# Kernel optimization log

Hardware: AMD Instinct MI355X
Metric: run time of the kernel (lower is better)

The kernel has to match this reference:

```python
import jax, jax.numpy as jnp
import numpy as np

N = 4096        # number of target nodes (also attention key length)
K = 10          # num_neighbors
E = 128         # embedding_dimension
EF = 64         # edge_feature_dim
T = 64          # time_encoding_dim
H = 2           # num_attention_heads
D = E + T       # query_dim = 192
KEY = E + EF + T            # per-neighbor key dim = 256
KD = KEY * K                # flattened kdim/vdim = 2560


def setup_inputs() -> dict:
    key = jax.random.key(0)
    ks = jax.random.split(key, 16)
    s = 0.02
    return {
        "features": jax.random.normal(ks[0], (N, E), jnp.float32),
        "edge_feats": jax.random.normal(ks[1], (N, K, EF), jnp.float32),
        "time_feats": jax.random.normal(ks[2], (N, K, T), jnp.float32),
        "neighbors": jax.random.randint(ks[3], (N, K), 0, N),
        "node_idx": jnp.arange(N),
        # MultiheadAttention projections (jax convention: x @ W + b, W is [in, out])
        "Wq": jax.random.normal(ks[4], (D, D), jnp.float32) * s,
        "bq": jnp.zeros((D,), jnp.float32),
        "Wk": jax.random.normal(ks[5], (KD, D), jnp.float32) * s,
        "bk": jnp.zeros((D,), jnp.float32),
        "Wv": jax.random.normal(ks[6], (KD, D), jnp.float32) * s,
        "bv": jnp.zeros((D,), jnp.float32),
        "Wo": jax.random.normal(ks[7], (D, D), jnp.float32) * s,
        "bo": jnp.zeros((D,), jnp.float32),
        # MLP([query_dim + embedding, embedding, embedding]) with ReLU between layers
        "W1": jax.random.normal(ks[8], (D + E, E), jnp.float32) * s,
        "b1": jnp.zeros((E,), jnp.float32),
        "W2": jax.random.normal(ks[9], (E, E), jnp.float32) * s,
        "b2": jnp.zeros((E,), jnp.float32),
    }


def reference(features, edge_feats, time_feats, neighbors, node_idx,
              Wq, bq, Wk, bk, Wv, bv, Wo, bo, W1, b1, W2, b2):
    n, k = neighbors.shape
    hd = D // H
    # _aggregate: gather neighbor node features, concat edge + time feats, flatten
    neigh = features[neighbors]                                       # [N, K, E]
    agg = jnp.concatenate([neigh, edge_feats, time_feats], axis=-1)   # [N, K, KEY]
    agg = agg.reshape(n, k * KEY)                                     # [N, KD]
    # query: node features padded with zero time encoding
    x = features[node_idx]                                            # [N, E]
    q_in = jnp.concatenate([x, jnp.zeros((n, T), features.dtype)], axis=-1)  # [N, D]
    # multi-head attention: batch=1, every query attends over all N aggregated keys
    q = (q_in @ Wq + bq).reshape(n, H, hd)
    kk = (agg @ Wk + bk).reshape(n, H, hd)
    vv = (agg @ Wv + bv).reshape(n, H, hd)
    scale = 1.0 / jnp.sqrt(jnp.asarray(hd, features.dtype))
    scores = jnp.einsum('nhd,mhd->hnm', q, kk) * scale                # [H, N, N]
    attn = jax.nn.softmax(scores, axis=-1)
    o = jnp.einsum('hnm,mhd->nhd', attn, vv).reshape(n, D)
    attn_out = o @ Wo + bo                                            # [N, D]
    # MLP over concat(node_feats, attn_out)
    h = jnp.concatenate([x, attn_out], axis=-1)                       # [N, D+E]
    return jax.nn.relu(h @ W1 + b1) @ W2 + b2                         # [N, E]
```

## Files before the change

kernel.cpp:

```cpp
#include <hip/hip_runtime.h>
#include <hip/hip_bf16.h>
#include <math.h>

#define NN   4096
#define KNB  10
#define ED   128
#define EFD  64
#define TD   64
#define DD   192
#define KEYD 256
#define KDD  2560
#define HD   96
#define NH   2
#define NSPLIT 4

typedef __attribute__((ext_vector_type(8))) short bf16x8;
typedef __attribute__((ext_vector_type(4))) float f32x4;
typedef __attribute__((ext_vector_type(2))) unsigned int u32x2;

__device__ inline short f2bf(float f) {
    union { float f; unsigned int u; } c; c.f = f;
    unsigned int r = (c.u + 0x7FFFu + ((c.u >> 16) & 1u)) >> 16;
    return (short)r;
}

__device__ inline float bf2f(short s) {
    union { unsigned int u; float f; } c;
    c.u = ((unsigned int)(unsigned short)s) << 16;
    return c.f;
}

__device__ inline void gload_lds16(const void* g, void* lds) {
    __builtin_amdgcn_global_load_lds(
        (const __attribute__((address_space(1))) void*)g,
        (__attribute__((address_space(3))) void*)lds, 16, 0, 0);
}

__global__ __launch_bounds__(256) void prep_convert(
    const float* __restrict__ Wk, const float* __restrict__ Wv,
    const float* __restrict__ Wq,
    const float* __restrict__ Wo, const float* __restrict__ bo,
    const float* __restrict__ W1, const float* __restrict__ b1,
    const float* __restrict__ W2,
    const float* __restrict__ features, const float* __restrict__ edge_feats,
    const float* __restrict__ time_feats, const int* __restrict__ node_idx,
    short* __restrict__ WkT, short* __restrict__ WvT, short* __restrict__ WqT,
    short* __restrict__ WcatT, short* __restrict__ W2T, float* __restrict__ bfold,
    short* __restrict__ featbf, short* __restrict__ xb,
    short* __restrict__ edgebf, short* __restrict__ timebf)
{
    int blk = blockIdx.x, t = threadIdx.x;
    if (blk < 254) {
        __shared__ float ts[64][65];
        const float* W; short* WT; int src_ld, dst_ld, k0, n0;
        if (blk < 240) {
            int z = blk / 120, r = blk % 120;
            W = z ? Wv : Wk; WT = z ? WvT : WkT;
            src_ld = DD; dst_ld = KDD; k0 = (r % 40) * 64; n0 = (r / 40) * 64;
        } else if (blk < 246) {
            int r = blk - 240;
            W = Wq; WT = WqT; src_ld = DD; dst_ld = ED;
            k0 = (r % 2) * 64; n0 = (r / 2) * 64;
        } else if (blk < 250) {
            int r = blk - 246;
            W = W1; WT = WcatT; src_ld = ED; dst_ld = 320;
            k0 = (r % 2) * 64; n0 = (r / 2) * 64;
        } else {
            int r = blk - 250;
            W = W2; WT = W2T; src_ld = ED; dst_ld = ED;
            k0 = (r % 2) * 64; n0 = (r / 2) * 64;
        }
        #pragma unroll
        for (int j = 0; j < 4; ++j) {
            int k = (t >> 4) + j * 16, n4 = (t & 15) * 4;
            float4 v = *(const float4*)&W[(size_t)(k0 + k) * src_ld + n0 + n4];
            ts[k][n4] = v.x; ts[k][n4 + 1] = v.y; ts[k][n4 + 2] = v.z; ts[k][n4 + 3] = v.w;
        }
        __syncthreads();
        int n = t >> 2, kc = (t & 3) * 16;
        short tmp[16];
        #pragma unroll
        for (int j = 0; j < 16; ++j) tmp[j] = f2bf(ts[kc + j][n]);
        *(bf16x8*)&WT[(size_t)(n0 + n) * dst_ld + k0 + kc] = *(bf16x8*)&tmp[0];
        *(bf16x8*)&WT[(size_t)(n0 + n) * dst_ld + k0 + kc + 8] = *(bf16x8*)&tmp[8];
    } else if (blk == 254) {
        if (t < 128) {
            float s = 0.f;
            for (int j = 0; j < DD; ++j) s += bo[j] * W1[(size_t)(ED + j) * ED + t];
            bfold[t] = s + b1[t];
        }
    } else if (blk < 447) {
        int d = blk - 255;
        if (t < 128) {
            float s = 0.f;
            for (int j = 0; j < DD; ++j)
                s += Wo[(size_t)d * DD + j] * W1[(size_t)(ED + j) * ED + t];
            WcatT[t * 320 + ED + d] = f2bf(s);
        }
    } else {
        int cb = blk - 447;
        if (cb < 512) {
            int e4 = cb * 256 + t;
            float4 v = *(const float4*)&features[(size_t)e4 * 4];
            short4 o; o.x = f2bf(v.x); o.y = f2bf(v.y); o.z = f2bf(v.z); o.w = f2bf(v.w);
            *(short4*)&featbf[(size_t)e4 * 4] = o;
        } else if (cb < 1024) {
            int l4 = (cb - 512) * 256 + t;
            int n = l4 >> 5, c = (l4 & 31) * 4;
            float4 v = *(const float4*)&features[(size_t)node_idx[n] * ED + c];
            short4 o; o.x = f2bf(v.x); o.y = f2bf(v.y); o.z = f2bf(v.z); o.w = f2bf(v.w);
            *(short4*)&xb[(size_t)n * ED + c] = o;
        } else if (cb < 3584) {
            int l4 = (cb - 1024) * 256 + t;
            float4 v = *(const float4*)&edge_feats[(size_t)l4 * 4];
            short4 o; o.x = f2bf(v.x); o.y = f2bf(v.y); o.z = f2bf(v.z); o.w = f2bf(v.w);
            *(short4*)&edgebf[(size_t)l4 * 4] = o;
        } else {
            int l4 = (cb - 3584) * 256 + t;
            float4 v = *(const float4*)&time_feats[(size_t)l4 * 4];
            short4 o; o.x = f2bf(v.x); o.y = f2bf(v.y); o.z = f2bf(v.z); o.w = f2bf(v.w);
            *(short4*)&timebf[(size_t)l4 * 4] = o;
        }
    }
}

__global__ __launch_bounds__(256) void kvq_gemm_mfma(
    const short* __restrict__ featbf, const short* __restrict__ edgebf,
    const short* __restrict__ timebf, const int* __restrict__ neighbors,
    const short* __restrict__ WkT, const short* __restrict__ WvT,
    short* __restrict__ psumK, short* __restrict__ psumV,
    const short* __restrict__ xb, const short* __restrict__ WqT,
    const float* __restrict__ bq, short* __restrict__ qb)
{
    __shared__ short As[2][128 * 64];
    __shared__ short Bs[2][2][64 * 64];
    __shared__ unsigned short nbr[128 * KNB];
    int tid = threadIdx.x, wid = tid >> 6, lane = tid & 63;
    int lx = lane & 15, lg = lane >> 4;
    int id = blockIdx.x;

    if (id < 384) {
        int xcd = id & 7, slot_ = id >> 3;
        int g = xcd * 16 + slot_ / 3;
        int nb = slot_ % 3;
        int mb = g >> 2, s = g & 3;
        int n0 = nb * 64;
        int m0 = mb * 128;
        int wm0 = (wid >> 1) * 64, wn0 = (wid & 1) * 32;

        for (int i = tid; i < 128 * KNB; i += 256)
            nbr[i] = (unsigned short)neighbors[(size_t)m0 * KNB + i];
        __syncthreads();

        f32x4 accK[4][2] = {}, accV[4][2] = {};

        auto stage = [&](int k0, int b) {
            #pragma unroll
            for (int it = 0; it < 4; ++it) {
                int idx = (wid * 4 + it) * 64 + lane;
                int m = idx >> 3, cs = (idx & 7) ^ (m & 7);
                int k = k0 + cs * 8;
                int slot = k >> 8, off = k & 255;
                int nbid = nbr[m * KNB + slot];
                const short* src;
                if (off < ED)
                    src = featbf + (size_t)nbid * ED + off;
                else if (off < ED + EFD)
                    src = edgebf + ((size_t)(m0 + m) * KNB + slot) * EFD + (off - ED);
                else
                    src = timebf + ((size_t)(m0 + m) * KNB + slot) * TD + (off - ED - EFD);
                gload_lds16(src, &As[b][(wid * 4 + it) * 512]);
            }
            #pragma unroll
            for (int it = 0; it < 2; ++it) {
                int idx = (wid * 2 + it) * 64 + lane;
                int n = idx >> 3, c = (idx & 7) ^ (n & 7);
                gload_lds16(WkT + (size_t)(n0 + n) * KDD + k0 + c * 8,
                            &Bs[b][0][(wid * 2 + it) * 512]);
            }
            #pragma unroll
            for (int it = 0; it < 2; ++it) {
                int idx = (wid * 2 + it) * 64 + lane;
                int n = idx >> 3, c = (idx & 7) ^ (n & 7);
                gload_lds16(WvT + (size_t)(n0 + n) * KDD + k0 + c * 8,
                            &Bs[b][1][(wid * 2 + it) * 512]);
            }
        };

        int kbase = s * (KDD / NSPLIT);
        stage(kbase, 0);
        for (int i = 0; i < 10; ++i) {
            int b = i & 1;
            __syncthreads();
            if (i < 9) stage(kbase + (i + 1) * 64, b ^ 1);
            #pragma unroll
            for (int ks = 0; ks < 2; ++ks) {
                bf16x8 af[4], bk8[2], bv8[2];
                #pragma unroll
                for (int mf = 0; mf < 4; ++mf) {
                    int m = wm0 + mf * 16 + lx;
                    af[mf] = *(const bf16x8*)&As[b][m * 64 + (((ks * 4 + lg) ^ (m & 7)) << 3)];
                }
                #pragma unroll
                for (int nf = 0; nf < 2; ++nf) {
                    int n = wn0 + nf * 16 + lx;
                    int o = n * 64 + (((ks * 4 + lg) ^ (n & 7)) << 3);
                    bk8[nf] = *(const bf16x8*)&Bs[b][0][o];
                    bv8[nf] = *(const bf16x8*)&Bs[b][1][o];
                }
                #pragma unroll
                for (int mf = 0; mf < 4; ++mf)
                    #pragma unroll
                    for (int nf = 0; nf < 2; ++nf) {
                        accK[mf][nf] = __builtin_amdgcn_mfma_f32_16x16x32_bf16(
                            af[mf], bk8[nf], accK[mf][nf], 0, 0, 0);
                        accV[mf][nf] = __builtin_amdgcn_mfma_f32_16x16x32_bf16(
                            af[mf], bv8[nf], accV[mf][nf], 0, 0, 0);
                    }
            }
        }
        #pragma unroll
        for (int nf = 0; nf < 2; ++nf) {
            int ncol = n0 + wn0 + nf * 16 + lx;
            #pragma unroll
            for (int mf = 0; mf < 4; ++mf) {
                int mrow = m0 + wm0 + mf * 16 + 4 * lg;
                #pragma unroll
                for (int r = 0; r < 4; ++r)
                    psumK[((size_t)s * NN + mrow + r) * DD + ncol] = f2bf(accK[mf][nf][r]);
                short4 s4;
                s4.x = f2bf(accV[mf][nf][0]); s4.y = f2bf(accV[mf][nf][1]);
                s4.z = f2bf(accV[mf][nf][2]); s4.w = f2bf(accV[mf][nf][3]);
                *(short4*)&psumV[((size_t)(s * DD + ncol)) * NN + mrow] = s4;
            }
        }
    } else {
        int qid = id - 384;
        int m0 = (qid / 3) * 64, n0 = (qid % 3) * 64;
        int wm0 = (wid >> 1) * 32, wn0 = (wid & 1) * 32;
        short* qAs = &As[0][0];
        short* qBs = &Bs[0][0][0];
        f32x4 acc[2][2] = {};

        for (int k0 = 0; k0 < ED; k0 += 64) {
            #pragma unroll
            for (int it = 0; it < 2; ++it) {
                int idx = (wid * 2 + it) * 64 + lane;
                int m = idx >> 3, c = (idx & 7) ^ (m & 7);
                gload_lds16(xb + (size_t)(m0 + m) * ED + k0 + c * 8, &qAs[(wid * 2 + it) * 512]);
            }
            #pragma unroll
            for (int it = 0; it < 2; ++it) {
                int idx = (wid * 2 + it) * 64 + lane;
                int n = idx >> 3, c = (idx & 7) ^ (n & 7);
                gload_lds16(WqT + (size_t)(n0 + n) * ED + k0 + c * 8, &qBs[(wid * 2 + it) * 512]);
            }
            __syncthreads();
            #pragma unroll
            for (int ks = 0; ks < 2; ++ks) {
                bf16x8 af[2], bfr[2];
                #pragma unroll
                for (int mf = 0; mf < 2; ++mf) {
                    int m = wm0 + mf * 16 + lx;
                    af[mf] = *(const bf16x8*)&qAs[m * 64 + (((ks * 4 + lg) ^ (m & 7)) << 3)];
                }
                #pragma unroll
                for (int nf = 0; nf < 2; ++nf) {
                    int n = wn0 + nf * 16 + lx;
                    bfr[nf] = *(const bf16x8*)&qBs[n * 64 + (((ks * 4 + lg) ^ (n & 7)) << 3)];
                }
                #pragma unroll
                for (int mf = 0; mf < 2; ++mf)
                    #pragma unroll
                    for (int nf = 0; nf < 2; ++nf)
                        acc[mf][nf] = __builtin_amdgcn_mfma_f32_16x16x32_bf16(
                            af[mf], bfr[nf], acc[mf][nf], 0, 0, 0);
            }
            __syncthreads();
        }
        const float scale = 0.10206207261596577f;
        #pragma unroll
        for (int nf = 0; nf < 2; ++nf) {
            int ncol = n0 + wn0 + nf * 16 + lx;
            float bb = bq[ncol];
            #pragma unroll
            for (int mf = 0; mf < 2; ++mf) {
                int mrow = m0 + wm0 + mf * 16 + 4 * lg;
                #pragma unroll
                for (int r = 0; r < 4; ++r)
                    qb[(size_t)(mrow + r) * DD + ncol] = f2bf((acc[mf][nf][r] + bb) * scale);
            }
        }
    }
}

__global__ __launch_bounds__(256) void kv_combine(
    const short* __restrict__ psumK, const short* __restrict__ psumV,
    const float* __restrict__ bk, const float* __restrict__ bv,
    short* __restrict__ kk, short* __restrict__ vvT)
{
    const int HALF = NN * DD / 4;
    int i = blockIdx.x * 256 + threadIdx.x;
    if (i < HALF) {
        int base = i * 4, n = base % DD;
        float sum[4] = {0.f, 0.f, 0.f, 0.f};
        #pragma unroll
        for (int s = 0; s < NSPLIT; ++s) {
            short4 v = *(const short4*)&psumK[(size_t)s * NN * DD + base];
            sum[0] += bf2f(v.x); sum[1] += bf2f(v.y);
            sum[2] += bf2f(v.z); sum[3] += bf2f(v.w);
        }
        float4 bb = *(const float4*)&bk[n];
        short4 o;
        o.x = f2bf(sum[0] + bb.x); o.y = f2bf(sum[1] + bb.y);
        o.z = f2bf(sum[2] + bb.z); o.w = f2bf(sum[3] + bb.w);
        *(short4*)&kk[base] = o;
    } else {
        int j = i - HALF;
        int base = j * 4, n = base / NN;
        float sum[4] = {0.f, 0.f, 0.f, 0.f};
        #pragma unroll
        for (int s = 0; s < NSPLIT; ++s) {
            short4 v = *(const short4*)&psumV[(size_t)s * DD * NN + base];
            sum[0] += bf2f(v.x); sum[1] += bf2f(v.y);
            sum[2] += bf2f(v.z); sum[3] += bf2f(v.w);
        }
        float bb = bv[n];
        short4 o;
        o.x = f2bf(sum[0] + bb); o.y = f2bf(sum[1] + bb);
        o.z = f2bf(sum[2] + bb); o.w = f2bf(sum[3] + bb);
        *(short4*)&vvT[base] = o;
    }
}

__global__ __launch_bounds__(512) void attn_mfma(
    const short* __restrict__ qb,
    const short* __restrict__ kk,
    const short* __restrict__ vvT,
    short* __restrict__ opart,
    float* __restrict__ ml)
{
    __shared__ short Ks[2][64 * 96];
    __shared__ short Vs[2][96 * 64];
    __shared__ short Ps[8][16 * 72];
    int tid = threadIdx.x, wid = tid >> 6, lane = tid & 63;
    int lx = lane & 15, lg = lane >> 4;
    int h = blockIdx.y, split = blockIdx.z;
    int hoff = h * HD;
    int qb0 = blockIdx.x * 128 + wid * 16;

    bf16x8 qf[3];
    #pragma unroll
    for (int ks = 0; ks < 3; ++ks)
        qf[ks] = *(const bf16x8*)&qb[(size_t)(qb0 + lx) * DD + hoff + ks * 32 + lg * 8];

    auto stage = [&](int kb, int b) {
        #pragma unroll
        for (int jj = 0; jj < 3; ++jj) {
            int j = wid * 3 + jj;
            if (j < 12) {
                int idx = j * 64 + lane;
                int row = idx / 12, c = idx % 12;
                gload_lds16(kk + (size_t)(kb + row) * DD + hoff + c * 8,
                            &Ks[b][j * 512]);
            } else {
                int idx = (j - 12) * 64 + lane;
                int d = idx >> 3, c = (idx & 7) ^ (d & 7);
                gload_lds16(vvT + (size_t)(hoff + d) * NN + kb + c * 8,
                            &Vs[b][(j - 12) * 512]);
            }
        }
    };

    float lsum = 0.0f;
    f32x4 accO[6] = {};
    short* myP = &Ps[wid][0];
    int kbase = split * (NN / NSPLIT);

    stage(kbase, 0);

    for (int t = 0; t < 16; ++t) {
        int b = t & 1;
        __syncthreads();
        if (t < 15) stage(kbase + (t + 1) * 64, b ^ 1);
        f32x4 sf[4];
        #pragma unroll
        for (int nf = 0; nf < 4; ++nf) sf[nf] = (f32x4){0.f, 0.f, 0.f, 0.f};
        #pragma unroll
        for (int ks = 0; ks < 3; ++ks) {
            #pragma unroll
            for (int nf = 0; nf < 4; ++nf) {
                bf16x8 kf = *(const bf16x8*)&Ks[b][(nf * 16 + lx) * 96 + ks * 32 + lg * 8];
                sf[nf] = __builtin_amdgcn_mfma_f32_16x16x32_bf16(kf, qf[ks], sf[nf], 0, 0, 0);
            }
        }
        #pragma unroll
        for (int nf = 0; nf < 4; ++nf) {
            float p0 = __expf(sf[nf][0]);
            float p1 = __expf(sf[nf][1]);
            float p2 = __expf(sf[nf][2]);
            float p3 = __expf(sf[nf][3]);
            lsum += (p0 + p1) + (p2 + p3);
            unsigned int u0, u1;
            asm("v_cvt_pk_bf16_f32 %0, %1, %2" : "=v"(u0) : "v"(p0), "v"(p1));
            asm("v_cvt_pk_bf16_f32 %0, %1, %2" : "=v"(u1) : "v"(p2), "v"(p3));
            *(u32x2*)&myP[lx * 72 + nf * 16 + 4 * lg] = (u32x2){u0, u1};
        }
        #pragma unroll
        for (int kf2 = 0; kf2 < 2; ++kf2) {
            bf16x8 pf = *(const bf16x8*)&myP[lx * 72 + kf2 * 32 + lg * 8];
            #pragma unroll
            for (int nf2 = 0; nf2 < 6; ++nf2) {
                int d = nf2 * 16 + lx;
                bf16x8 vf = *(const bf16x8*)&Vs[b][d * 64 + (((kf2 * 4 + lg) ^ (d & 7)) << 3)];
                accO[nf2] = __builtin_amdgcn_mfma_f32_16x16x32_bf16(pf, vf, accO[nf2], 0, 0, 0);
            }
        }
    }

    short* op = opart + ((size_t)split * NN + qb0) * DD + hoff;
    #pragma unroll
    for (int nf2 = 0; nf2 < 6; ++nf2)
        #pragma unroll
        for (int r = 0; r < 4; ++r)
            op[(size_t)(4 * lg + r) * DD + nf2 * 16 + lx] = f2bf(accO[nf2][r]);
    lsum += __shfl_xor(lsum, 16);
    lsum += __shfl_xor(lsum, 32);
    if (lane < 16)
        ml[((size_t)(split * NH + h)) * NN + qb0 + lx] = lsum;
}

__global__ __launch_bounds__(256) void mlp_fused(
    const short* __restrict__ xb,
    const short* __restrict__ opart,
    const float* __restrict__ ml,
    const short* __restrict__ WcatT,
    const float* __restrict__ bfold,
    const short* __restrict__ W2T,
    const float* __restrict__ b2,
    float* __restrict__ out)
{
    __shared__ short As[16 * 64];
    __shared__ short Bs[128 * 64];
    __shared__ short Ts[16 * 128];
    __shared__ float linv[32];
    int tid = threadIdx.x, wid = tid >> 6, lane = tid & 63;
    int lx = lane & 15, lg = lane >> 4;
    int m0 = blockIdx.x * 16;
    int wn0 = wid * 32;

    if (tid < 32) {
        int rl = tid >> 1, hh = tid & 1;
        float l = 0.f;
        #pragma unroll
        for (int s = 0; s < NSPLIT; ++s) l += ml[(size_t)(s * NH + hh) * NN + m0 + rl];
        linv[tid] = 1.0f / l;
    }

    f32x4 acc[2] = {};
    for (int step = 0; step < 5; ++step) {
        int k0 = step * 64;
        if (step < 2) {
            if (wid < 2) {
                int idx = tid;
                int m = idx >> 3, c = (idx & 7) ^ (m & 7);
                gload_lds16(xb + (size_t)(m0 + m) * ED + k0 + c * 8, &As[wid * 512]);
            }
        } else {
            if (tid < 128) {
                int m = tid >> 3, j8 = tid & 7;
                int dg = (k0 - 128) + j8 * 8;
                float sum[8] = {};
                #pragma unroll
                for (int s = 0; s < NSPLIT; ++s) {
                    bf16x8 v = *(const bf16x8*)&opart[((size_t)s * NN + m0 + m) * DD + dg];
                    #pragma unroll
                    for (int j = 0; j < 8; ++j) sum[j] += bf2f(v[j]);
                }
                float inv = linv[m * 2 + (dg >= HD ? 1 : 0)];
                short tmp[8];
                #pragma unroll
                for (int j = 0; j < 8; ++j) tmp[j] = f2bf(sum[j] * inv);
                *(bf16x8*)&As[m * 64 + ((j8 ^ (m & 7)) << 3)] = *(bf16x8*)&tmp[0];
            }
        }
        #pragma unroll
        for (int it = 0; it < 4; ++it) {
            int idx = (wid * 4 + it) * 64 + lane;
            int n = idx >> 3, c = (idx & 7) ^ (n & 7);
            gload_lds16(WcatT + (size_t)n * 320 + k0 + c * 8, &Bs[(wid * 4 + it) * 512]);
        }
        __syncthreads();
        #pragma unroll
        for (int kss = 0; kss < 2; ++kss) {
            int m = lx;
            bf16x8 af = *(const bf16x8*)&As[m * 64 + (((kss * 4 + lg) ^ (m & 7)) << 3)];
            #pragma unroll
            for (int nf = 0; nf < 2; ++nf) {
                int n = wn0 + nf * 16 + lx;
                bf16x8 bfr = *(const bf16x8*)&Bs[n * 64 + (((kss * 4 + lg) ^ (n & 7)) << 3)];
                acc[nf] = __builtin_amdgcn_mfma_f32_16x16x32_bf16(af, bfr, acc[nf], 0, 0, 0);
            }
        }
        __syncthreads();
    }
    #pragma unroll
    for (int nf = 0; nf < 2; ++nf) {
        int kcol = wn0 + nf * 16 + lx;
        float bb = bfold[kcol];
        #pragma unroll
        for (int r = 0; r < 4; ++r) {
            int m = 4 * lg + r;
            float v = fmaxf(acc[nf][r] + bb, 0.f);
            Ts[m * 128 + ((((kcol >> 3) ^ (m & 7)) << 3) | (kcol & 7))] = f2bf(v);
        }
    }
    __syncthreads();
    f32x4 acc2[2] = {};
    #pragma unroll
    for (int step = 0; step < 2; ++step) {
        int k0 = step * 64;
        #pragma unroll
        for (int it = 0; it < 4; ++it) {
            int idx = (wid * 4 + it) * 64 + lane;
            int n = idx >> 3, c = (idx & 7) ^ (n & 7);
            gload_lds16(W2T + (size_t)n * 128 + k0 + c * 8, &Bs[(wid * 4 + it) * 512]);
        }
        __syncthreads();
        #pragma unroll
        for (int kss = 0; kss < 2; ++kss) {
            int m = lx;
            int chunk = step * 8 + kss * 4 + lg;
            bf16x8 af = *(const bf16x8*)&Ts[m * 128 + ((chunk ^ (m & 7)) << 3)];
            #pragma unroll
            for (int nf = 0; nf < 2; ++nf) {
                int n = wn0 + nf * 16 + lx;
                bf16x8 bfr = *(const bf16x8*)&Bs[n * 64 + (((kss * 4 + lg) ^ (n & 7)) << 3)];
                acc2[nf] = __builtin_amdgcn_mfma_f32_16x16x32_bf16(af, bfr, acc2[nf], 0, 0, 0);
            }
        }
        __syncthreads();
    }
    #pragma unroll
    for (int nf = 0; nf < 2; ++nf) {
        int ncol = wn0 + nf * 16 + lx;
        float bb = b2[ncol];
        #pragma unroll
        for (int r = 0; r < 4; ++r)
            out[(size_t)(m0 + 4 * lg + r) * 128 + ncol] = acc2[nf][r] + bb;
    }
}

extern "C" void kernel_launch(void* const* d_in, const int* in_sizes, int n_in,
                              void* d_out, int out_size, void* d_ws, size_t ws_size,
                              hipStream_t stream) {
    const float* features   = (const float*)d_in[0];
    const float* edge_feats = (const float*)d_in[1];
    const float* time_feats = (const float*)d_in[2];
    const int*   neighbors  = (const int*)d_in[3];
    const int*   node_idx   = (const int*)d_in[4];
    const float* Wq = (const float*)d_in[5];
    const float* bq = (const float*)d_in[6];
    const float* Wk = (const float*)d_in[7];
    const float* bk = (const float*)d_in[8];
    const float* Wv = (const float*)d_in[9];
    const float* bv = (const float*)d_in[10];
    const float* Wo = (const float*)d_in[11];
    const float* bo = (const float*)d_in[12];
    const float* W1 = (const float*)d_in[13];
    const float* b1 = (const float*)d_in[14];
    const float* W2 = (const float*)d_in[15];
    const float* b2 = (const float*)d_in[16];
    float* out = (float*)d_out;

    char* w = (char*)d_ws;
    short* featbf = (short*)w;  w += (size_t)NN * ED * 2;
    short* xb     = (short*)w;  w += (size_t)NN * ED * 2;
    short* edgebf = (short*)w;  w += (size_t)NN * KNB * EFD * 2;
    short* timebf = (short*)w;  w += (size_t)NN * KNB * TD * 2;
    short* qb     = (short*)w;  w += (size_t)NN * DD * 2;
    short* kkb    = (short*)w;  w += (size_t)NN * DD * 2;
    short* vvT    = (short*)w;  w += (size_t)DD * NN * 2;
    short* WkT    = (short*)w;  w += (size_t)DD * KDD * 2;
    short* WvT    = (short*)w;  w += (size_t)DD * KDD * 2;
    short* WqT    = (short*)w;  w += (size_t)DD * ED * 2;
    short* WcatT  = (short*)w;  w += (size_t)ED * 320 * 2;
    short* W2T    = (short*)w;  w += (size_t)ED * ED * 2;
    float* bfold  = (float*)w;  w += (size_t)ED * 4;
    short* psumK = (short*)w;
    short* psumV = psumK + (size_t)NSPLIT * NN * DD;
    short* opart = (short*)w;
    float* ml    = (float*)(opart + (size_t)NSPLIT * NN * DD);

    prep_convert<<<6591, 256, 0, stream>>>(
        Wk, Wv, Wq, Wo, bo, W1, b1, W2,
        features, edge_feats, time_feats, node_idx,
        WkT, WvT, WqT, WcatT, W2T, bfold, featbf, xb, edgebf, timebf);
    kvq_gemm_mfma<<<384 + 192, 256, 0, stream>>>(
        featbf, edgebf, timebf, neighbors, WkT, WvT, psumK, psumV, xb, WqT, bq, qb);
    kv_combine<<<2 * NN * DD / 4 / 256, 256, 0, stream>>>(psumK, psumV, bk, bv, kkb, vvT);
    attn_mfma<<<dim3(NN / 128, NH, NSPLIT), 512, 0, stream>>>(qb, kkb, vvT, opart, ml);
    mlp_fused<<<NN / 16, 256, 0, stream>>>(xb, opart, ml, WcatT, bfold, W2T, b2, out);
}
```

Before: 67.43 us.

## Fuse KV combine, attention and MLP into one persistent kernel with grid barriers

```diff
diff --git a/kernel.cpp b/kernel.cpp
--- a/kernel.cpp
+++ b/kernel.cpp
@@ -36,6 +36,22 @@
         (__attribute__((address_space(3))) void*)lds, 16, 0, 0);
 }
 
+__device__ inline void grid_barrier(unsigned* cnt, unsigned* gen, unsigned nblk) {
+    __syncthreads();
+    __threadfence();
+    if (threadIdx.x == 0) {
+        unsigned g = atomicAdd(gen, 0u);
+        if (atomicAdd(cnt, 1u) == nblk - 1) {
+            atomicExch(cnt, 0u);
+            atomicAdd(gen, 1u);
+        } else {
+            while (atomicAdd(gen, 0u) == g) { __builtin_amdgcn_s_sleep(2); }
+        }
+    }
+    __threadfence();
+    __syncthreads();
+}
+
 __global__ __launch_bounds__(256) void prep_convert(
     const float* __restrict__ Wk, const float* __restrict__ Wv,
     const float* __restrict__ Wq,
@@ -47,7 +63,8 @@
     short* __restrict__ WkT, short* __restrict__ WvT, short* __restrict__ WqT,
     short* __restrict__ WcatT, short* __restrict__ W2T, float* __restrict__ bfold,
     short* __restrict__ featbf, short* __restrict__ xb,
-    short* __restrict__ edgebf, short* __restrict__ timebf)
+    short* __restrict__ edgebf, short* __restrict__ timebf,
+    unsigned* __restrict__ syncb)
 {
     int blk = blockIdx.x, t = threadIdx.x;
     if (blk < 254) {
@@ -88,6 +105,8 @@
             float s = 0.f;
             for (int j = 0; j < DD; ++j) s += bo[j] * W1[(size_t)(ED + j) * ED + t];
             bfold[t] = s + b1[t];
+        } else if (t < 132) {
+            syncb[t - 128] = 0u;
         }
     } else if (blk < 447) {
         int d = blk - 255;
@@ -294,260 +313,274 @@
     }
 }
 
-__global__ __launch_bounds__(256) void kv_combine(
+__global__ __launch_bounds__(512) void fused_tail(
     const short* __restrict__ psumK, const short* __restrict__ psumV,
     const float* __restrict__ bk, const float* __restrict__ bv,
-    short* __restrict__ kk, short* __restrict__ vvT)
+    short* __restrict__ kk, short* __restrict__ vvT,
+    const short* __restrict__ qb,
+    short* __restrict__ opart, float* __restrict__ ml,
+    const short* __restrict__ xb,
+    const short* __restrict__ WcatT, const float* __restrict__ bfold,
+    const short* __restrict__ W2T, const float* __restrict__ b2,
+    float* __restrict__ out,
+    unsigned* __restrict__ syncb)
 {
-    const int HALF = NN * DD / 4;
-    int i = blockIdx.x * 256 + threadIdx.x;
-    if (i < HALF) {
-        int base = i * 4, n = base % DD;
-        float sum[4] = {0.f, 0.f, 0.f, 0.f};
-        #pragma unroll
-        for (int s = 0; s < NSPLIT; ++s) {
-            short4 v = *(const short4*)&psumK[(size_t)s * NN * DD + base];
-            sum[0] += bf2f(v.x); sum[1] += bf2f(v.y);
-            sum[2] += bf2f(v.z); sum[3] += bf2f(v.w);
-        }
-        float4 bb = *(const float4*)&bk[n];
-        short4 o;
-        o.x = f2bf(sum[0] + bb.x); o.y = f2bf(sum[1] + bb.y);
-        o.z = f2bf(sum[2] + bb.z); o.w = f2bf(sum[3] + bb.w);
-        *(short4*)&kk[base] = o;
-    } else {
-        int j = i - HALF;
-        int base = j * 4, n = base / NN;
-        float sum[4] = {0.f, 0.f, 0.f, 0.f};
-        #pragma unroll
-        for (int s = 0; s < NSPLIT; ++s) {
-            short4 v = *(const short4*)&psumV[(size_t)s * DD * NN + base];
-            sum[0] += bf2f(v.x); sum[1] += bf2f(v.y);
-            sum[2] += bf2f(v.z); sum[3] += bf2f(v.w);
-        }
-        float bb = bv[n];
-        short4 o;
-        o.x = f2bf(sum[0] + bb); o.y = f2bf(sum[1] + bb);
-        o.z = f2bf(sum[2] + bb); o.w = f2bf(sum[3] + bb);
-        *(short4*)&vvT[base] = o;
-    }
-}
-
-__global__ __launch_bounds__(512) void attn_mfma(
-    const short* __restrict__ qb,
-    const short* __restrict__ kk,
-    const short* __restrict__ vvT,
-    short* __restrict__ opart,
-    float* __restrict__ ml)
-{
-    __shared__ short Ks[2][64 * 96];
-    __shared__ short Vs[2][96 * 64];
-    __shared__ short Ps[8][16 * 72];
+    __shared__ __align__(16) char smem[67584];
     int tid = threadIdx.x, wid = tid >> 6, lane = tid & 63;
     int lx = lane & 15, lg = lane >> 4;
-    int h = blockIdx.y, split = blockIdx.z;
-    int hoff = h * HD;
-    int qb0 = blockIdx.x * 128 + wid * 16;
-
-    bf16x8 qf[3];
-    #pragma unroll
-    for (int ks = 0; ks < 3; ++ks)
-        qf[ks] = *(const bf16x8*)&qb[(size_t)(qb0 + lx) * DD + hoff + ks * 32 + lg * 8];
-
-    auto stage = [&](int kb, int b) {
-        #pragma unroll
-        for (int jj = 0; jj < 3; ++jj) {
-            int j = wid * 3 + jj;
-            if (j < 12) {
-                int idx = j * 64 + lane;
-                int row = idx / 12, c = idx % 12;
-                gload_lds16(kk + (size_t)(kb + row) * DD + hoff + c * 8,
-                            &Ks[b][j * 512]);
+    int bid = blockIdx.x;
+    const int HALF = NN * DD / 4;
+
+    {
+        int gtid = bid * 512 + tid;
+        #pragma unroll
+        for (int it = 0; it < 3; ++it) {
+            int i = gtid + it * 131072;
+            if (i < HALF) {
+                int base = i * 4, n = base % DD;
+                float sum[4] = {0.f, 0.f, 0.f, 0.f};
+                #pragma unroll
+                for (int s = 0; s < NSPLIT; ++s) {
+                    short4 v = *(const short4*)&psumK[(size_t)s * NN * DD + base];
+                    sum[0] += bf2f(v.x); sum[1] += bf2f(v.y);
+                    sum[2] += bf2f(v.z); sum[3] += bf2f(v.w);
+                }
+                float4 bb = *(const float4*)&bk[n];
+                short4 o;
+                o.x = f2bf(sum[0] + bb.x); o.y = f2bf(sum[1] + bb.y);
+                o.z = f2bf(sum[2] + bb.z); o.w = f2bf(sum[3] + bb.w);
+                *(short4*)&kk[base] = o;
             } else {
-                int idx = (j - 12) * 64 + lane;
-                int d = idx >> 3, c = (idx & 7) ^ (d & 7);
-                gload_lds16(vvT + (size_t)(hoff + d) * NN + kb + c * 8,
-                            &Vs[b][(j - 12) * 512]);
-            }
-        }
-    };
-
-    float lsum = 0.0f;
-    f32x4 accO[6] = {};
-    short* myP = &Ps[wid][0];
-    int kbase = split * (NN / NSPLIT);
-
-    stage(kbase, 0);
-
-    for (int t = 0; t < 16; ++t) {
-        int b = t & 1;
+                int j = i - HALF;
+                int base = j * 4, n = base / NN;
+                float sum[4] = {0.f, 0.f, 0.f, 0.f};
+                #pragma unroll
+                for (int s = 0; s < NSPLIT; ++s) {
+                    short4 v = *(const short4*)&psumV[(size_t)s * DD * NN + base];
+                    sum[0] += bf2f(v.x); sum[1] += bf2f(v.y);
+                    sum[2] += bf2f(v.z); sum[3] += bf2f(v.w);
+                }
+                float bb = bv[n];
+                short4 o;
+                o.x = f2bf(sum[0] + bb); o.y = f2bf(sum[1] + bb);
+                o.z = f2bf(sum[2] + bb); o.w = f2bf(sum[3] + bb);
+                *(short4*)&vvT[base] = o;
+            }
+        }
+    }
+    grid_barrier(&syncb[0], &syncb[1], 256);
+
+    {
+        short* Ks = (short*)smem;
+        short* Vs = (short*)(smem + 24576);
+        short* Ps = (short*)(smem + 49152);
+        int bx = bid & 31, h = (bid >> 5) & 1, split = bid >> 6;
+        int hoff = h * HD;
+        int qb0 = bx * 128 + wid * 16;
+
+        bf16x8 qf[3];
+        #pragma unroll
+        for (int ks = 0; ks < 3; ++ks)
+            qf[ks] = *(const bf16x8*)&qb[(size_t)(qb0 + lx) * DD + hoff + ks * 32 + lg * 8];
+
+        auto stage = [&](int kb, int b) {
+            #pragma unroll
+            for (int jj = 0; jj < 3; ++jj) {
+                int j = wid * 3 + jj;
+                if (j < 12) {
+                    int idx = j * 64 + lane;
+                    int row = idx / 12, c = idx % 12;
+                    gload_lds16(kk + (size_t)(kb + row) * DD + hoff + c * 8,
+                                &Ks[b * 6144 + j * 512]);
+                } else {
+                    int idx = (j - 12) * 64 + lane;
+                    int d = idx >> 3, c = (idx & 7) ^ (d & 7);
+                    gload_lds16(vvT + (size_t)(hoff + d) * NN + kb + c * 8,
+                                &Vs[b * 6144 + (j - 12) * 512]);
+                }
+            }
+        };
+
+        float lsum = 0.0f;
+        f32x4 accO[6] = {};
+        short* myP = &Ps[wid * 1152];
+        int kbase = split * (NN / NSPLIT);
+
+        stage(kbase, 0);
+
+        for (int t = 0; t < 16; ++t) {
+            int b = t & 1;
+            __syncthreads();
+            if (t < 15) stage(kbase + (t + 1) * 64, b ^ 1);
+            f32x4 sf[4];
+            #pragma unroll
+            for (int nf = 0; nf < 4; ++nf) sf[nf] = (f32x4){0.f, 0.f, 0.f, 0.f};
+            #pragma unroll
+            for (int ks = 0; ks < 3; ++ks) {
+                #pragma unroll
+                for (int nf = 0; nf < 4; ++nf) {
+                    bf16x8 kf = *(const bf16x8*)&Ks[b * 6144 + (nf * 16 + lx) * 96 + ks * 32 + lg * 8];
+                    sf[nf] = __builtin_amdgcn_mfma_f32_16x16x32_bf16(kf, qf[ks], sf[nf], 0, 0, 0);
+                }
+            }
+            #pragma unroll
+            for (int nf = 0; nf < 4; ++nf) {
+                float p0 = __expf(sf[nf][0]);
+                float p1 = __expf(sf[nf][1]);
+                float p2 = __expf(sf[nf][2]);
+                float p3 = __expf(sf[nf][3]);
+                lsum += (p0 + p1) + (p2 + p3);
+                unsigned int u0, u1;
+                asm("v_cvt_pk_bf16_f32 %0, %1, %2" : "=v"(u0) : "v"(p0), "v"(p1));
+                asm("v_cvt_pk_bf16_f32 %0, %1, %2" : "=v"(u1) : "v"(p2), "v"(p3));
+                *(u32x2*)&myP[lx * 72 + nf * 16 + 4 * lg] = (u32x2){u0, u1};
+            }
+            #pragma unroll
+            for (int kf2 = 0; kf2 < 2; ++kf2) {
+                bf16x8 pf = *(const bf16x8*)&myP[lx * 72 + kf2 * 32 + lg * 8];
+                #pragma unroll
+                for (int nf2 = 0; nf2 < 6; ++nf2) {
+                    int d = nf2 * 16 + lx;
+                    bf16x8 vf = *(const bf16x8*)&Vs[b * 6144 + d * 64 + (((kf2 * 4 + lg) ^ (d & 7)) << 3)];
+                    accO[nf2] = __builtin_amdgcn_mfma_f32_16x16x32_bf16(pf, vf, accO[nf2], 0, 0, 0);
+                }
+            }
+        }
+
+        short* op = opart + ((size_t)split * NN + qb0) * DD + hoff;
+        #pragma unroll
+        for (int nf2 = 0; nf2 < 6; ++nf2)
+            #pragma unroll
+            for (int r = 0; r < 4; ++r)
+                op[(size_t)(4 * lg + r) * DD + nf2 * 16 + lx] = f2bf(accO[nf2][r]);
+        lsum += __shfl_xor(lsum, 16);
+        lsum += __shfl_xor(lsum, 32);
+        if (lane < 16)
+            ml[((size_t)(split * NH + h)) * NN + qb0 + lx] = lsum;
+    }
+    grid_barrier(&syncb[2], &syncb[3], 256);
+
+    {
+        short* As = (short*)smem;
+        short* Bs = (short*)(smem + 2048);
+        short* Ts = (short*)(smem + 18432);
+        float* linv = (float*)(smem + 22528);
+        int m0 = bid * 16;
+        bool act = tid < 256;
+        int wn0 = wid * 32;
+
+        if (tid < 32) {
+            int rl = tid >> 1, hh = tid & 1;
+            float l = 0.f;
+            #pragma unroll
+            for (int s = 0; s < NSPLIT; ++s) l += ml[(size_t)(s * NH + hh) * NN + m0 + rl];
+            linv[tid] = 1.0f / l;
+        }
+
+        f32x4 acc[2] = {};
+        for (int step = 0; step < 5; ++step) {
+            int k0 = step * 64;
+            if (step < 2) {
+                if (wid < 2) {
+                    int idx = tid;
+                    int m = idx >> 3, c = (idx & 7) ^ (m & 7);
+                    gload_lds16(xb + (size_t)(m0 + m) * ED + k0 + c * 8, &As[wid * 512]);
+                }
+            } else {
+                if (act && tid < 128) {
+                    int m = tid >> 3, j8 = tid & 7;
+                    int dg = (k0 - 128) + j8 * 8;
+                    float sum[8] = {};
+                    #pragma unroll
+                    for (int s = 0; s < NSPLIT; ++s) {
+                        bf16x8 v = *(const bf16x8*)&opart[((size_t)s * NN + m0 + m) * DD + dg];
+                        #pragma unroll
+                        for (int j = 0; j < 8; ++j) sum[j] += bf2f(v[j]);
+                    }
+                    float inv = linv[m * 2 + (dg >= HD ? 1 : 0)];
+                    short tmp[8];
+                    #pragma unroll
+                    for (int j = 0; j < 8; ++j) tmp[j] = f2bf(sum[j] * inv);
+                    *(bf16x8*)&As[m * 64 + ((j8 ^ (m & 7)) << 3)] = *(bf16x8*)&tmp[0];
+                }
+            }
+            if (act) {
+                #pragma unroll
+                for (int it = 0; it < 4; ++it) {
+                    int idx = (wid * 4 + it) * 64 + lane;
+                    int n = idx >> 3, c = (idx & 7) ^ (n & 7);
+                    gload_lds16(WcatT + (size_t)n * 320 + k0 + c * 8, &Bs[(wid * 4 + it) * 512]);
+                }
+            }
+            __syncthreads();
+            if (act) {
+                #pragma unroll
+                for (int kss = 0; kss < 2; ++kss) {
+                    int m = lx;
+                    bf16x8 af = *(const bf16x8*)&As[m * 64 + (((kss * 4 + lg) ^ (m & 7)) << 3)];
+                    #pragma unroll
+                    for (int nf = 0; nf < 2; ++nf) {
+                        int n = wn0 + nf * 16 + lx;
+                        bf16x8 bfr = *(const bf16x8*)&Bs[n * 64 + (((kss * 4 + lg) ^ (n & 7)) << 3)];
+                        acc[nf] = __builtin_amdgcn_mfma_f32_16x16x32_bf16(af, bfr, acc[nf], 0, 0, 0);
+                    }
+                }
+            }
+            __syncthreads();
+        }
+        if (act) {
+            #pragma unroll
+            for (int nf = 0; nf < 2; ++nf) {
+                int kcol = wn0 + nf * 16 + lx;
+                float bb = bfold[kcol];
+                #pragma unroll
+                for (int r = 0; r < 4; ++r) {
+                    int m = 4 * lg + r;
+                    float v = fmaxf(acc[nf][r] + bb, 0.f);
+                    Ts[m * 128 + ((((kcol >> 3) ^ (m & 7)) << 3) | (kcol & 7))] = f2bf(v);
+                }
+            }
+        }
         __syncthreads();
-        if (t < 15) stage(kbase + (t + 1) * 64, b ^ 1);
-        f32x4 sf[4];
-        #pragma unroll
-        for (int nf = 0; nf < 4; ++nf) sf[nf] = (f32x4){0.f, 0.f, 0.f, 0.f};
-        #pragma unroll
-        for (int ks = 0; ks < 3; ++ks) {
-            #pragma unroll
-            for (int nf = 0; nf < 4; ++nf) {
-                bf16x8 kf = *(const bf16x8*)&Ks[b][(nf * 16 + lx) * 96 + ks * 32 + lg * 8];
-                sf[nf] = __builtin_amdgcn_mfma_f32_16x16x32_bf16(kf, qf[ks], sf[nf], 0, 0, 0);
-            }
-        }
-        #pragma unroll
-        for (int nf = 0; nf < 4; ++nf) {
-            float p0 = __expf(sf[nf][0]);
-            float p1 = __expf(sf[nf][1]);
-            float p2 = __expf(sf[nf][2]);
-            float p3 = __expf(sf[nf][3]);
-            lsum += (p0 + p1) + (p2 + p3);
-            unsigned int u0, u1;
-            asm("v_cvt_pk_bf16_f32 %0, %1, %2" : "=v"(u0) : "v"(p0), "v"(p1));
-            asm("v_cvt_pk_bf16_f32 %0, %1, %2" : "=v"(u1) : "v"(p2), "v"(p3));
-            *(u32x2*)&myP[lx * 72 + nf * 16 + 4 * lg] = (u32x2){u0, u1};
-        }
-        #pragma unroll
-        for (int kf2 = 0; kf2 < 2; ++kf2) {
-            bf16x8 pf = *(const bf16x8*)&myP[lx * 72 + kf2 * 32 + lg * 8];
-            #pragma unroll
-            for (int nf2 = 0; nf2 < 6; ++nf2) {
-                int d = nf2 * 16 + lx;
-                bf16x8 vf = *(const bf16x8*)&Vs[b][d * 64 + (((kf2 * 4 + lg) ^ (d & 7)) << 3)];
-                accO[nf2] = __builtin_amdgcn_mfma_f32_16x16x32_bf16(pf, vf, accO[nf2], 0, 0, 0);
-            }
-        }
-    }
-
-    short* op = opart + ((size_t)split * NN + qb0) * DD + hoff;
-    #pragma unroll
-    for (int nf2 = 0; nf2 < 6; ++nf2)
-        #pragma unroll
-        for (int r = 0; r < 4; ++r)
-            op[(size_t)(4 * lg + r) * DD + nf2 * 16 + lx] = f2bf(accO[nf2][r]);
-    lsum += __shfl_xor(lsum, 16);
-    lsum += __shfl_xor(lsum, 32);
-    if (lane < 16)
-        ml[((size_t)(split * NH + h)) * NN + qb0 + lx] = lsum;
-}
-
-__global__ __launch_bounds__(256) void mlp_fused(
-    const short* __restrict__ xb,
-    const short* __restrict__ opart,
-    const float* __restrict__ ml,
-    const short* __restrict__ WcatT,
-    const float* __restrict__ bfold,
-    const short* __restrict__ W2T,
-    const float* __restrict__ b2,
-    float* __restrict__ out)
-{
-    __shared__ short As[16 * 64];
-    __shared__ short Bs[128 * 64];
-    __shared__ short Ts[16 * 128];
-    __shared__ float linv[32];
-    int tid = threadIdx.x, wid = tid >> 6, lane = tid & 63;
-    int lx = lane & 15, lg = lane >> 4;
-    int m0 = blockIdx.x * 16;
-    int wn0 = wid * 32;
-
-    if (tid < 32) {
-        int rl = tid >> 1, hh = tid & 1;
-        float l = 0.f;
-        #pragma unroll
-        for (int s = 0; s < NSPLIT; ++s) l += ml[(size_t)(s * NH + hh) * NN + m0 + rl];
-        linv[tid] = 1.0f / l;
-    }
-
-    f32x4 acc[2] = {};
-    for (int step = 0; step < 5; ++step) {
-        int k0 = step * 64;
-        if (step < 2) {
-            if (wid < 2) {
-                int idx = tid;
-                int m = idx >> 3, c = (idx & 7) ^ (m & 7);
-                gload_lds16(xb + (size_t)(m0 + m) * ED + k0 + c * 8, &As[wid * 512]);
-            }
-        } else {
-            if (tid < 128) {
-                int m = tid >> 3, j8 = tid & 7;
-                int dg = (k0 - 128) + j8 * 8;
-                float sum[8] = {};
-                #pragma unroll
-                for (int s = 0; s < NSPLIT; ++s) {
-                    bf16x8 v = *(const bf16x8*)&opart[((size_t)s * NN + m0 + m) * DD + dg];
+        f32x4 acc2[2] = {};
+        #pragma unroll
+        for (int step = 0; step < 2; ++step) {
+            int k0 = step * 64;
+            if (act) {
+                #pragma unroll
+                for (int it = 0; it < 4; ++it) {
+                    int idx = (wid * 4 + it) * 64 + lane;
+                    int n = idx >> 3, c = (idx & 7) ^ (n & 7);
+                    gload_lds16(W2T + (size_t)n * 128 + k0 + c * 8, &Bs[(wid * 4 + it) * 512]);
+                }
+            }
+            __syncthreads();
+            if (act) {
+                #pragma unroll
+                for (int kss = 0; kss < 2; ++kss) {
+                    int m = lx;
+                    int chunk = step * 8 + kss * 4 + lg;
+                    bf16x8 af = *(const bf16x8*)&Ts[m * 128 + ((chunk ^ (m & 7)) << 3)];
                     #pragma unroll
-                    for (int j = 0; j < 8; ++j) sum[j] += bf2f(v[j]);
-                }
-                float inv = linv[m * 2 + (dg >= HD ? 1 : 0)];
-                short tmp[8];
-                #pragma unroll
-                for (int j = 0; j < 8; ++j) tmp[j] = f2bf(sum[j] * inv);
-                *(bf16x8*)&As[m * 64 + ((j8 ^ (m & 7)) << 3)] = *(bf16x8*)&tmp[0];
-            }
-        }
-        #pragma unroll
-        for (int it = 0; it < 4; ++it) {
-            int idx = (wid * 4 + it) * 64 + lane;
-            int n = idx >> 3, c = (idx & 7) ^ (n & 7);
-            gload_lds16(WcatT + (size_t)n * 320 + k0 + c * 8, &Bs[(wid * 4 + it) * 512]);
-        }
-        __syncthreads();
-        #pragma unroll
-        for (int kss = 0; kss < 2; ++kss) {
-            int m = lx;
-            bf16x8 af = *(const bf16x8*)&As[m * 64 + (((kss * 4 + lg) ^ (m & 7)) << 3)];
+                    for (int nf = 0; nf < 2; ++nf) {
+                        int n = wn0 + nf * 16 + lx;
+                        bf16x8 bfr = *(const bf16x8*)&Bs[n * 64 + (((kss * 4 + lg) ^ (n & 7)) << 3)];
+                        acc2[nf] = __builtin_amdgcn_mfma_f32_16x16x32_bf16(af, bfr, acc2[nf], 0, 0, 0);
+                    }
+                }
+            }
+            __syncthreads();
+        }
+        if (act) {
             #pragma unroll
             for (int nf = 0; nf < 2; ++nf) {
-                int n = wn0 + nf * 16 + lx;
-                bf16x8 bfr = *(const bf16x8*)&Bs[n * 64 + (((kss * 4 + lg) ^ (n & 7)) << 3)];
-                acc[nf] = __builtin_amdgcn_mfma_f32_16x16x32_bf16(af, bfr, acc[nf], 0, 0, 0);
-            }
-        }
-        __syncthreads();
-    }
-    #pragma unroll
-    for (int nf = 0; nf < 2; ++nf) {
-        int kcol = wn0 + nf * 16 + lx;
-        float bb = bfold[kcol];
-        #pragma unroll
-        for (int r = 0; r < 4; ++r) {
-            int m = 4 * lg + r;
-            float v = fmaxf(acc[nf][r] + bb, 0.f);
-            Ts[m * 128 + ((((kcol >> 3) ^ (m & 7)) << 3) | (kcol & 7))] = f2bf(v);
-        }
-    }
-    __syncthreads();
-    f32x4 acc2[2] = {};
-    #pragma unroll
-    for (int step = 0; step < 2; ++step) {
-        int k0 = step * 64;
-        #pragma unroll
-        for (int it = 0; it < 4; ++it) {
-            int idx = (wid * 4 + it) * 64 + lane;
-            int n = idx >> 3, c = (idx & 7) ^ (n & 7);
-            gload_lds16(W2T + (size_t)n * 128 + k0 + c * 8, &Bs[(wid * 4 + it) * 512]);
-        }
-        __syncthreads();
-        #pragma unroll
-        for (int kss = 0; kss < 2; ++kss) {
-            int m = lx;
-            int chunk = step * 8 + kss * 4 + lg;
-            bf16x8 af = *(const bf16x8*)&Ts[m * 128 + ((chunk ^ (m & 7)) << 3)];
-            #pragma unroll
-            for (int nf = 0; nf < 2; ++nf) {
-                int n = wn0 + nf * 16 + lx;
-                bf16x8 bfr = *(const bf16x8*)&Bs[n * 64 + (((kss * 4 + lg) ^ (n & 7)) << 3)];
-                acc2[nf] = __builtin_amdgcn_mfma_f32_16x16x32_bf16(af, bfr, acc2[nf], 0, 0, 0);
-            }
-        }
-        __syncthreads();
-    }
-    #pragma unroll
-    for (int nf = 0; nf < 2; ++nf) {
-        int ncol = wn0 + nf * 16 + lx;
-        float bb = b2[ncol];
-        #pragma unroll
-        for (int r = 0; r < 4; ++r)
-            out[(size_t)(m0 + 4 * lg + r) * 128 + ncol] = acc2[nf][r] + bb;
+                int ncol = wn0 + nf * 16 + lx;
+                float bb = b2[ncol];
+                #pragma unroll
+                for (int r = 0; r < 4; ++r)
+                    out[(size_t)(m0 + 4 * lg + r) * 128 + ncol] = acc2[nf][r] + bb;
+            }
+        }
     }
 }
 
@@ -587,6 +620,7 @@
     short* WcatT  = (short*)w;  w += (size_t)ED * 320 * 2;
     short* W2T    = (short*)w;  w += (size_t)ED * ED * 2;
     float* bfold  = (float*)w;  w += (size_t)ED * 4;
+    unsigned* syncb = (unsigned*)w;  w += 16;
     short* psumK = (short*)w;
     short* psumV = psumK + (size_t)NSPLIT * NN * DD;
     short* opart = (short*)w;
@@ -595,10 +629,10 @@
     prep_convert<<<6591, 256, 0, stream>>>(
         Wk, Wv, Wq, Wo, bo, W1, b1, W2,
         features, edge_feats, time_feats, node_idx,
-        WkT, WvT, WqT, WcatT, W2T, bfold, featbf, xb, edgebf, timebf);
+        WkT, WvT, WqT, WcatT, W2T, bfold, featbf, xb, edgebf, timebf, syncb);
     kvq_gemm_mfma<<<384 + 192, 256, 0, stream>>>(
         featbf, edgebf, timebf, neighbors, WkT, WvT, psumK, psumV, xb, WqT, bq, qb);
-    kv_combine<<<2 * NN * DD / 4 / 256, 256, 0, stream>>>(psumK, psumV, bk, bv, kkb, vvT);
-    attn_mfma<<<dim3(NN / 128, NH, NSPLIT), 512, 0, stream>>>(qb, kkb, vvT, opart, ml);
-    mlp_fused<<<NN / 16, 256, 0, stream>>>(xb, opart, ml, WcatT, bfold, W2T, b2, out);
-}
+    fused_tail<<<256, 512, 0, stream>>>(
+        psumK, psumV, bk, bv, kkb, vvT, qb, opart, ml,
+        xb, WcatT, bfold, W2T, b2, out, syncb);
+}
```

New measurement: 218.6 us. +224.2%, slower.
